# Optimization experiments

Measured on AMD Instinct MI355X. Metric: run time of the kernel, lower is better.

Reference implementation:

```python
import jax, jax.numpy as jnp
import numpy as np


def _div_tree_level(n_agents, level):
    # Deterministic reproduction of get_division_tree (seeded shuffle), row `level`.
    rng = np.random.RandomState(0)
    perm = rng.permutation(n_agents)
    max_div = int(np.ceil(np.log2(n_agents)))
    levels = np.zeros((max_div + 1, n_agents), dtype=np.int64)
    for ith in range(1, max_div + 1):
        levels[ith] = levels[ith - 1]
        for j in range(n_agents):
            seg = j // (n_agents / 2 ** ith)
            if int(seg) % 2 == 1:
                levels[ith, j] += 2 ** (ith - 1)
    res = levels[:, perm]  # res_levels[:, i] = levels[:, agent2divitreeindex[i]]
    return res[level]


def setup_inputs() -> dict:
    B, A, D, H, NA = 4096, 32, 512, 512, 32
    LEVEL = 3  # current_level after change_div_tree_level(3): 8 distinct experts
    key = jax.random.key(0)
    ks = jax.random.split(key, 4)
    x0 = jax.random.normal(ks[0], (B, A, D), dtype=jnp.float32)
    W_shared = jax.random.normal(ks[1], (D, H), dtype=jnp.float32) * 0.02
    b_shared = jnp.zeros((H,), jnp.float32)
    W1 = jax.random.normal(ks[2], (A, H, H), dtype=jnp.float32) * 0.02
    b1 = jnp.zeros((A, H), jnp.float32)
    W2 = jax.random.normal(ks[3], (A, H, NA), dtype=jnp.float32) * 0.02
    b2 = jnp.zeros((A, NA), jnp.float32)
    route = jnp.asarray(_div_tree_level(A, LEVEL), dtype=jnp.int32)  # [A] expert id per agent
    return dict(x0=x0, W_shared=W_shared, b_shared=b_shared,
                W1=W1, b1=b1, W2=W2, b2=b2, route=route)


def reference(x0, W_shared, b_shared, W1, b1, W2, b2, route):
    # shared trunk: Linear + ReLU over all agents at once
    x1 = jax.nn.relu(x0 @ W_shared + b_shared)          # [B, A, H]
    # static MoE dispatch: gather each agent's expert weights, batched GEMM per agent slot
    Wg1, bg1 = W1[route], b1[route]                     # [A, H, H], [A, H]
    Wg2, bg2 = W2[route], b2[route]                     # [A, H, NA], [A, NA]
    h = jax.nn.relu(jnp.einsum('bah,ahk->bak', x1, Wg1) + bg1)   # [B, A, H]
    x2 = jnp.einsum('bah,ahk->bak', h, Wg2) + bg2       # [B, A, NA]
    return x2
```

## Files before the change

kernel.cpp:

```cpp
#include <hip/hip_runtime.h>
#include <cstdint>
#include <cstddef>

typedef __bf16 bf16x8 __attribute__((ext_vector_type(8)));
typedef float f32x4 __attribute__((ext_vector_type(4)));
typedef unsigned short u16;
typedef u16 u16x4 __attribute__((ext_vector_type(4)));
typedef u16 u16x8 __attribute__((ext_vector_type(8)));

__device__ __forceinline__ u16 f2bf(float f) {
  union { float f; unsigned u; } v; v.f = f;
  return (u16)((v.u + 0x7FFFu + ((v.u >> 16) & 1u)) >> 16);
}

__device__ __forceinline__ void cvt_wr(u16* dst, float4 v) {
  const u16x4 d = { f2bf(v.x), f2bf(v.y), f2bf(v.z), f2bf(v.w) };
  *(u16x4*)dst = d;
}

__device__ __forceinline__ float4 ntld(const float* p) {
  f32x4 v = __builtin_nontemporal_load((const f32x4*)p);
  union { f32x4 a; float4 b; } u; u.a = v;
  return u.b;
}

__global__ void frag_cvt(const float* __restrict__ in, const int* __restrict__ sel,
                         u16* __restrict__ out, int K, int N) {
  const int s = blockIdx.z;
  if (sel) {
    bool need = false;
#pragma unroll
    for (int i = 0; i < 32; ++i) need |= (sel[i] == s);
    if (!need) return;
  }
  const int f = threadIdx.x >> 6, l = threadIdx.x & 63;
  const int r = l & 15, q = l >> 4;
  const int kt = blockIdx.x * 4 + f;
  const int nb = blockIdx.y;
  const int KT = K >> 5, NB = N >> 4;
  const float* ip = in + (size_t)s * K * N + (size_t)(kt * 32 + q * 8) * N + nb * 16 + r;
  u16x8 d;
#pragma unroll
  for (int e = 0; e < 8; ++e) d[e] = f2bf(ip[(size_t)e * N]);
  *(u16x8*)&out[((((size_t)s * NB + nb) * KT + kt) * 64 + l) * 8] = d;
}

__device__ __forceinline__ void epi_relu(u16* __restrict__ Xs, const float* __restrict__ bias,
                                         f32x4 acc[8][2], int wn, int r, int q) {
#pragma unroll
  for (int mt = 0; mt < 8; ++mt) {
#pragma unroll
    for (int nt = 0; nt < 2; ++nt) {
      const int col = wn * 32 + nt * 16 + q * 4;
      const int q2 = (col >> 3) & 3;
      const float4 bb = *(const float4*)&bias[col];
      const f32x4 v = acc[mt][nt];
      const u16x4 d = { f2bf(fmaxf(v.x + bb.x, 0.f)), f2bf(fmaxf(v.y + bb.y, 0.f)),
                        f2bf(fmaxf(v.z + bb.z, 0.f)), f2bf(fmaxf(v.w + bb.w, 0.f)) };
      *(u16x4*)&Xs[((wn * 8 + mt) * 64 + q2 * 16 + r) * 8 + (q & 1) * 4] = d;
    }
  }
}

__global__ __launch_bounds__(1024, 4)
void fused_mlp(const float* __restrict__ X0, const u16* __restrict__ Wsf,
               const float* __restrict__ bsh, const u16* __restrict__ W1f,
               const float* __restrict__ b1, const u16* __restrict__ W2f,
               const float* __restrict__ b2, const int* __restrict__ route,
               float* __restrict__ Out) {
  __shared__ u16 Xs[65536];

  const int tid = threadIdx.x;
  const int w = tid >> 6, l = tid & 63;
  const int r = l & 15, q = l >> 4;
  const int wn = w;

  const int bid = blockIdx.x;
  const int xcd = bid & 7, idx = bid >> 3;
  const int a = (xcd << 2) | (idx >> 5);
  const int b0 = (idx & 31) << 7;
  const int rt = route[a];

  const int sm = tid >> 3, scq = tid & 7;
  const float* gx = X0 + (((size_t)(b0 + sm) * 32 + a) << 9) + (scq << 2);
  const int sdst = (((sm >> 4) << 6) + ((scq >> 1) << 4) + (sm & 15)) * 8 + (scq & 1) * 4;

  const u16* Af = Xs + l * 8;

  f32x4 acc[8][2];
#pragma unroll
  for (int mt = 0; mt < 8; ++mt)
#pragma unroll
    for (int nt = 0; nt < 2; ++nt) acc[mt][nt] = (f32x4){0.f, 0.f, 0.f, 0.f};

  float4 vb[4];
  vb[0] = ntld(gx);
  vb[1] = ntld(gx + 32);
  vb[2] = ntld(gx + 64);
  vb[3] = ntld(gx + 96);
  cvt_wr(&Xs[sdst], vb[0]);
  __syncthreads();

  {
    const float* gxc = gx + 128;
    const u16* Bw0 = Wsf + (wn << 14) + l * 8;
    const u16* Bw1 = Bw0 + 8192;
    u16* Xw = Xs + sdst + 4096;
#pragma unroll 1
    for (int c = 0; c < 4; ++c) {
#pragma unroll
      for (int u = 0; u < 4; ++u) {
        if (c < 3) vb[u] = ntld(gxc + u * 32);
        const bf16x8 bc0 = *(const bf16x8*)(Bw0 + u * 512);
        const bf16x8 bc1 = *(const bf16x8*)(Bw1 + u * 512);
#pragma unroll
        for (int mt = 0; mt < 8; ++mt) {
          const bf16x8 af = *(const bf16x8*)(Af + (c * 16384 + u * 4096) + mt * 512);
          acc[mt][0] = __builtin_amdgcn_mfma_f32_16x16x32_bf16(bc0, af, acc[mt][0], 0, 0, 0);
          acc[mt][1] = __builtin_amdgcn_mfma_f32_16x16x32_bf16(bc1, af, acc[mt][1], 0, 0, 0);
        }
        if (u < 3 || c < 3) {
          cvt_wr(Xw + u * 4096, vb[(u + 1) & 3]);
          __syncthreads();
        }
      }
      gxc += 128; Bw0 += 2048; Bw1 += 2048; Xw += 16384;
    }
  }
  __syncthreads();

  const u16* B1 = W1f + ((size_t)rt << 18) + (wn << 14) + l * 8;
  bf16x8 bc0 = *(const bf16x8*)(B1);
  bf16x8 bc1 = *(const bf16x8*)(B1 + 8192);

  epi_relu(Xs, bsh, acc, wn, r, q);
  __syncthreads();

#pragma unroll
  for (int mt = 0; mt < 8; ++mt)
#pragma unroll
    for (int nt = 0; nt < 2; ++nt) acc[mt][nt] = (f32x4){0.f, 0.f, 0.f, 0.f};
  {
    const u16* B1c = B1;
#pragma unroll 1
    for (int c = 0; c < 4; ++c) {
#pragma unroll
      for (int u = 0; u < 4; ++u) {
        bf16x8 bn0, bn1;
        const bool pf = (u < 3) || (c < 3);
        if (pf) {
          bn0 = *(const bf16x8*)(B1c + (u + 1) * 512);
          bn1 = *(const bf16x8*)(B1c + 8192 + (u + 1) * 512);
        }
#pragma unroll
        for (int mt = 0; mt < 8; ++mt) {
          const bf16x8 af = *(const bf16x8*)(Af + (c * 16384 + u * 4096) + mt * 512);
          acc[mt][0] = __builtin_amdgcn_mfma_f32_16x16x32_bf16(bc0, af, acc[mt][0], 0, 0, 0);
          acc[mt][1] = __builtin_amdgcn_mfma_f32_16x16x32_bf16(bc1, af, acc[mt][1], 0, 0, 0);
        }
        if (pf) { bc0 = bn0; bc1 = bn1; }
      }
      B1c += 2048;
    }
  }
  __syncthreads();
  epi_relu(Xs, b1 + (size_t)rt * 512, acc, wn, r, q);
  __syncthreads();

  {
    const int mtg = w >> 1, nt3 = w & 1;
    const u16* Ah = Xs + (mtg << 9) + l * 8;
    const u16* B2 = W2f + ((size_t)rt << 14) + (nt3 << 13) + l * 8;
    f32x4 o = (f32x4){0.f, 0.f, 0.f, 0.f};
#pragma unroll 1
    for (int c = 0; c < 4; ++c) {
#pragma unroll
      for (int u = 0; u < 4; ++u) {
        const bf16x8 af = *(const bf16x8*)(Ah + (c * 16384 + u * 4096));
        const bf16x8 bf = *(const bf16x8*)(B2 + u * 512);
        o = __builtin_amdgcn_mfma_f32_16x16x32_bf16(bf, af, o, 0, 0, 0);
      }
      B2 += 2048;
    }
    const int col = (nt3 << 4) + (q << 2);
    const float4 bb = *(const float4*)&b2[rt * 32 + col];
    const float4 res = { o.x + bb.x, o.y + bb.y, o.z + bb.z, o.w + bb.w };
    *(float4*)&Out[(size_t)(b0 + (mtg << 4) + r) * 1024 + a * 32 + col] = res;
  }
}

extern "C" void kernel_launch(void* const* d_in, const int* in_sizes, int n_in,
                              void* d_out, int out_size, void* d_ws, size_t ws_size,
                              hipStream_t stream) {
  (void)in_sizes; (void)n_in; (void)out_size; (void)ws_size;
  const float* x0  = (const float*)d_in[0];
  const float* Wsh = (const float*)d_in[1];
  const float* bsh = (const float*)d_in[2];
  const float* W1  = (const float*)d_in[3];
  const float* b1  = (const float*)d_in[4];
  const float* W2  = (const float*)d_in[5];
  const float* b2  = (const float*)d_in[6];
  const int* route = (const int*)d_in[7];
  float* out = (float*)d_out;

  char* ws = (char*)d_ws;
  u16* Wsf = (u16*)(ws + 0);
  u16* W1f = (u16*)(ws + 524288);
  u16* W2f = (u16*)(ws + 524288 + 16777216);

  frag_cvt<<<dim3(4, 32, 1),  256, 0, stream>>>(Wsh, nullptr, Wsf, 512, 512);
  frag_cvt<<<dim3(4, 32, 32), 256, 0, stream>>>(W1, route, W1f, 512, 512);
  frag_cvt<<<dim3(4, 2, 32),  256, 0, stream>>>(W2, route, W2f, 512, 32);
  fused_mlp<<<dim3(1024), 1024, 0, stream>>>(x0, Wsf, bsh, W1f, b1, W2f, b2, route, out);
}
```

Baseline: 520.2 us.

## Restage shared-trunk GEMM to load X in 128-wide chunks with one barrier each

The shared-trunk loop now converts and stores a full 128-column chunk of X0 into LDS before each group of four k-steps. This replaces a barrier after every k-step with one barrier per chunk. It also software-prefetches the next Wsh fragments in registers, as the second GEMM already does. The LDS pointer arithmetic is strength-reduced, and the final output store becomes nontemporal. The trade is more registers held for the prefetched values and a deeper global-load prefetch distance, which could affect occupancy.

Result: slower. 572.7 us (+10.1%).

```diff
diff --git a/kernel.cpp b/kernel.cpp
--- a/kernel.cpp
+++ b/kernel.cpp
@@ -22,6 +22,10 @@
   f32x4 v = __builtin_nontemporal_load((const f32x4*)p);
   union { f32x4 a; float4 b; } u; u.a = v;
   return u.b;
+}
+__device__ __forceinline__ void ntst(float* p, float4 v) {
+  union { f32x4 a; float4 b; } u; u.b = v;
+  __builtin_nontemporal_store(u.a, (f32x4*)p);
 }
 
 __global__ void frag_cvt(const float* __restrict__ in, const int* __restrict__ sel,
@@ -99,32 +103,46 @@
   vb[2] = ntld(gx + 64);
   vb[3] = ntld(gx + 96);
   cvt_wr(&Xs[sdst], vb[0]);
+  cvt_wr(&Xs[sdst + 4096], vb[1]);
+  cvt_wr(&Xs[sdst + 8192], vb[2]);
+  cvt_wr(&Xs[sdst + 12288], vb[3]);
   __syncthreads();
 
   {
-    const float* gxc = gx + 128;
-    const u16* Bw0 = Wsf + (wn << 14) + l * 8;
-    const u16* Bw1 = Bw0 + 8192;
-    u16* Xw = Xs + sdst + 4096;
+    const float* gxt = gx + 128;
+    const u16* Bw = Wsf + (wn << 14) + l * 8;
+    u16* Xw = Xs + sdst + 16384;
+    const u16* Aft = Af;
+    bf16x8 bc0 = *(const bf16x8*)(Bw);
+    bf16x8 bc1 = *(const bf16x8*)(Bw + 8192);
 #pragma unroll 1
-    for (int c = 0; c < 4; ++c) {
+    for (int t = 0; t < 4; ++t) {
+      if (t < 3) {
+#pragma unroll
+        for (int u = 0; u < 4; ++u) vb[u] = ntld(gxt + u * 32);
+      }
 #pragma unroll
       for (int u = 0; u < 4; ++u) {
-        if (c < 3) vb[u] = ntld(gxc + u * 32);
-        const bf16x8 bc0 = *(const bf16x8*)(Bw0 + u * 512);
-        const bf16x8 bc1 = *(const bf16x8*)(Bw1 + u * 512);
+        bf16x8 bn0, bn1;
+        const bool pf = (u < 3) || (t < 3);
+        if (pf) {
+          bn0 = *(const bf16x8*)(Bw + (u + 1) * 512);
+          bn1 = *(const bf16x8*)(Bw + 8192 + (u + 1) * 512);
+        }
 #pragma unroll
         for (int mt = 0; mt < 8; ++mt) {
-          const bf16x8 af = *(const bf16x8*)(Af + (c * 16384 + u * 4096) + mt * 512);
+          const bf16x8 af = *(const bf16x8*)(Aft + u * 4096 + mt * 512);
           acc[mt][0] = __builtin_amdgcn_mfma_f32_16x16x32_bf16(bc0, af, acc[mt][0], 0, 0, 0);
           acc[mt][1] = __builtin_amdgcn_mfma_f32_16x16x32_bf16(bc1, af, acc[mt][1], 0, 0, 0);
         }
-        if (u < 3 || c < 3) {
-          cvt_wr(Xw + u * 4096, vb[(u + 1) & 3]);
-          __syncthreads();
-        }
-      }
-      gxc += 128; Bw0 += 2048; Bw1 += 2048; Xw += 16384;
+        if (pf) { bc0 = bn0; bc1 = bn1; }
+      }
+      if (t < 3) {
+#pragma unroll
+        for (int u = 0; u < 4; ++u) cvt_wr(Xw + u * 4096, vb[u]);
+        __syncthreads();
+      }
+      gxt += 128; Bw += 2048; Xw += 16384; Aft += 16384;
     }
   }
   __syncthreads();
@@ -142,6 +160,7 @@
     for (int nt = 0; nt < 2; ++nt) acc[mt][nt] = (f32x4){0.f, 0.f, 0.f, 0.f};
   {
     const u16* B1c = B1;
+    const u16* Afc = Af;
 #pragma unroll 1
     for (int c = 0; c < 4; ++c) {
 #pragma unroll
@@ -154,13 +173,13 @@
         }
 #pragma unroll
         for (int mt = 0; mt < 8; ++mt) {
-          const bf16x8 af = *(const bf16x8*)(Af + (c * 16384 + u * 4096) + mt * 512);
+          const bf16x8 af = *(const bf16x8*)(Afc + u * 4096 + mt * 512);
           acc[mt][0] = __builtin_amdgcn_mfma_f32_16x16x32_bf16(bc0, af, acc[mt][0], 0, 0, 0);
           acc[mt][1] = __builtin_amdgcn_mfma_f32_16x16x32_bf16(bc1, af, acc[mt][1], 0, 0, 0);
         }
         if (pf) { bc0 = bn0; bc1 = bn1; }
       }
-      B1c += 2048;
+      B1c += 2048; Afc += 16384;
     }
   }
   __syncthreads();
@@ -185,7 +204,7 @@
     const int col = (nt3 << 4) + (q << 2);
     const float4 bb = *(const float4*)&b2[rt * 32 + col];
     const float4 res = { o.x + bb.x, o.y + bb.y, o.z + bb.z, o.w + bb.w };
-    *(float4*)&Out[(size_t)(b0 + (mtg << 4) + r) * 1024 + a * 32 + col] = res;
+    ntst(&Out[(size_t)(b0 + (mtg << 4) + r) * 1024 + a * 32 + col], res);
   }
 }
 
```
